# Kernel optimization log

Measured on AMD Instinct MI355X. Metric: run time of the kernel, lower is better.

Reference implementation:

```python
import jax, jax.numpy as jnp
import numpy as np

N_AUTHOR, N_PAPER = 20000, 50000
E = 300000
D, H = 256, 8
DK = D // H  # 32


def setup_inputs() -> dict:
    key = jax.random.key(0)
    ks = jax.random.split(key, 20)
    s = np.float32(1.0 / np.sqrt(D))
    sr = np.float32(1.0 / np.sqrt(DK))
    inp = {
        "h_author": jax.random.normal(ks[0], (N_AUTHOR, D), jnp.float32),
        "h_paper": jax.random.normal(ks[1], (N_PAPER, D), jnp.float32),
        "k_w": jax.random.normal(ks[2], (2, D, D), jnp.float32) * s,
        "k_b": jnp.zeros((2, D), jnp.float32),
        "q_w": jax.random.normal(ks[3], (2, D, D), jnp.float32) * s,
        "q_b": jnp.zeros((2, D), jnp.float32),
        "v_w": jax.random.normal(ks[4], (2, D, D), jnp.float32) * s,
        "v_b": jnp.zeros((2, D), jnp.float32),
        "a_w": jax.random.normal(ks[5], (2, D, D), jnp.float32) * s,
        "a_b": jnp.zeros((2, D), jnp.float32),
        "rel_att": jax.random.normal(ks[6], (3, H, DK, DK), jnp.float32) * sr,
        "rel_msg": jax.random.normal(ks[7], (3, H, DK, DK), jnp.float32) * sr,
        "rel_pri": jnp.ones((3, H), jnp.float32),
        "skip": jnp.ones((2,), jnp.float32),
        "src_writes": jax.random.randint(ks[8], (E,), 0, N_AUTHOR),
        "dst_writes": jax.random.randint(ks[9], (E,), 0, N_PAPER),
        "src_cites": jax.random.randint(ks[10], (E,), 0, N_PAPER),
        "dst_cites": jax.random.randint(ks[11], (E,), 0, N_PAPER),
        "src_wb": jax.random.randint(ks[12], (E,), 0, N_PAPER),
        "dst_wb": jax.random.randint(ks[13], (E,), 0, N_AUTHOR),
    }
    return inp


def _seg_softmax(score, seg, n):
    # dst-normalized edge softmax (per-etype subgraph, like DGL edge_softmax)
    m = jax.ops.segment_max(score, seg, num_segments=n)
    m = jnp.where(jnp.isfinite(m), m, 0.0)
    a = jnp.exp(score - m[seg])
    s = jax.ops.segment_sum(a, seg, num_segments=n)
    return a / s[seg]


def _etype_agg(h_src, h_dst, kw, kb, qw, qb, vw, vb, ratt, rmsg, pri, src, dst, n_dst):
    k = (h_src @ kw.T + kb).reshape(-1, H, DK)
    v = (h_src @ vw.T + vb).reshape(-1, H, DK)
    q = (h_dst @ qw.T + qb).reshape(-1, H, DK)
    k = jnp.einsum('nhi,hij->nhj', k, ratt)
    v = jnp.einsum('nhi,hij->nhj', v, rmsg)
    score = (q[dst] * k[src]).sum(-1) * pri / np.float32(np.sqrt(DK))  # [E,H]
    attn = _seg_softmax(score, dst, n_dst)
    return jax.ops.segment_sum(v[src] * attn[:, :, None], dst, num_segments=n_dst)


def reference(h_author, h_paper, k_w, k_b, q_w, q_b, v_w, v_b, a_w, a_b,
              rel_att, rel_msg, rel_pri, skip,
              src_writes, dst_writes, src_cites, dst_cites, src_wb, dst_wb):
    # ntypes: author=0, paper=1; etypes: writes=0 (a->p), cites=1 (p->p), written_by=2 (p->a)
    agg_p = _etype_agg(h_author, h_paper, k_w[0], k_b[0], q_w[1], q_b[1], v_w[0], v_b[0],
                       rel_att[0], rel_msg[0], rel_pri[0], src_writes, dst_writes, N_PAPER)
    agg_p = agg_p + _etype_agg(h_paper, h_paper, k_w[1], k_b[1], q_w[1], q_b[1], v_w[1], v_b[1],
                               rel_att[1], rel_msg[1], rel_pri[1], src_cites, dst_cites, N_PAPER)
    agg_a = _etype_agg(h_paper, h_author, k_w[1], k_b[1], q_w[0], q_b[0], v_w[1], v_b[1],
                       rel_att[2], rel_msg[2], rel_pri[2], src_wb, dst_wb, N_AUTHOR)

    def out_block(agg, h, nid):
        alpha = jax.nn.sigmoid(skip[nid])
        trans = agg.reshape(-1, D) @ a_w[nid].T + a_b[nid]
        return trans * alpha + h * (1.0 - alpha)

    return (out_block(agg_a, h_author, 0), out_block(agg_p, h_paper, 1))
```

## Files before the change

### kernel.cpp

```cpp
#include <hip/hip_runtime.h>
#include <hip/hip_bf16.h>

#define NA 20000
#define NP 50000
#define NE 300000
#define DD 256
#define HH 8
#define NTOT (2 * NP + NA)
#define NBLK ((NTOT + 2047) / 2048)
#define NRT 391

typedef short bf16x8 __attribute__((ext_vector_type(8)));
typedef float f32x4 __attribute__((ext_vector_type(4)));

__device__ __forceinline__ float b2f(ushort u) {
  unsigned v = ((unsigned)u) << 16;
  float f;
  __builtin_memcpy(&f, &v, 4);
  return f;
}
__device__ __forceinline__ float b2f_lo(int u) {
  unsigned v = ((unsigned)u) << 16;
  float f;
  __builtin_memcpy(&f, &v, 4);
  return f;
}
__device__ __forceinline__ float b2f_hi(int u) {
  unsigned v = ((unsigned)u) & 0xffff0000u;
  float f;
  __builtin_memcpy(&f, &v, 4);
  return f;
}
__device__ __forceinline__ ushort f2b(float f) {
  unsigned u;
  __builtin_memcpy(&u, &f, 4);
  u = u + 0x7fffu + ((u >> 16) & 1u);
  return (ushort)(u >> 16);
}
__device__ __forceinline__ unsigned pk2(float lo, float hi) {
  return (unsigned)f2b(lo) | ((unsigned)f2b(hi) << 16);
}
__device__ __forceinline__ float ldf(const void* p, int i, int isbf) {
  return isbf ? b2f(((const ushort*)p)[i]) : ((const float*)p)[i];
}
__device__ __forceinline__ int get_isbf(const void* rpri) {
  return ((const unsigned*)rpri)[0] == 0x3F803F80u;
}
__device__ __forceinline__ void gload16(const void* g, void* l) {
  __builtin_amdgcn_global_load_lds(
      (const __attribute__((address_space(1))) void*)g,
      (__attribute__((address_space(3))) void*)l, 16, 0, 0);
}

__global__ __launch_bounds__(256) void cvt_h(const void* __restrict__ ha,
                                             const void* __restrict__ hp,
                                             ushort* __restrict__ Ha,
                                             ushort* __restrict__ Hp,
                                             const void* __restrict__ rpri) {
  int isbf = get_isbf(rpri);
  size_t t = (size_t)blockIdx.x * 256 + threadIdx.x;
  const size_t nA = (size_t)NA * 256 / 8;
  const size_t nT = nA + (size_t)NP * 256 / 8;
  if (t >= nT) return;
  const void* src;
  ushort* dst;
  size_t o;
  if (t < nA) { src = ha; dst = Ha; o = t * 8; }
  else        { src = hp; dst = Hp; o = (t - nA) * 8; }
  if (isbf) {
    *(int4*)(dst + o) = *(const int4*)((const ushort*)src + o);
  } else {
    const float* f = (const float*)src + o;
    float4 x = *(const float4*)f;
    float4 y = *(const float4*)(f + 4);
    int4 v;
    v.x = (int)pk2(x.x, x.y); v.y = (int)pk2(x.z, x.w);
    v.z = (int)pk2(y.x, y.y); v.w = (int)pk2(y.z, y.w);
    *(int4*)(dst + o) = v;
  }
}

__global__ __launch_bounds__(256) void prep(const void* __restrict__ q_w,
                                            const void* __restrict__ a_w,
                                            const void* __restrict__ k_w,
                                            const void* __restrict__ v_w,
                                            const void* __restrict__ k_b,
                                            const void* __restrict__ v_b,
                                            const void* __restrict__ q_b,
                                            const void* __restrict__ ratt,
                                            const void* __restrict__ rmsg,
                                            ushort* __restrict__ Bp,
                                            ushort* __restrict__ Ba,
                                            ushort* __restrict__ aeff,
                                            float* __restrict__ gb,
                                            const void* __restrict__ rpri) {
  int isbf = get_isbf(rpri);
  int y = blockIdx.y;
  int r = blockIdx.x;
  int c = threadIdx.x;
  if (y < 3) {
    int e = y;
    int nt = (e == 2) ? 0 : 1;
    int h = r >> 5, i = r & 31;
    int rb = ((e * HH + h) * 32 + i) * 32;
    int qb = nt * 65536 + (h * 32) * 256 + c;
    float s = 0.f;
#pragma unroll 8
    for (int j = 0; j < 32; j++) s += ldf(ratt, rb + j, isbf) * ldf(q_w, qb + j * 256, isbf);
    ushort* dst = (e == 2) ? (Ba + (size_t)(512 + r) * 256)
                           : (Bp + (size_t)(512 + e * 256 + r) * 256);
    dst[c] = f2b(s);
  } else if (y < 6) {
    int e = y - 3;
    int o = r;
    int nt = (e == 2) ? 0 : 1;
    int h = c >> 5, i = c & 31;
    int rb = ((e * HH + h) * 32 + i) * 32;
    int ab = nt * 65536 + o * 256 + h * 32;
    float s = 0.f;
#pragma unroll 8
    for (int j = 0; j < 32; j++) s += ldf(rmsg, rb + j, isbf) * ldf(a_w, ab + j, isbf);
    aeff[(e * 256 + o) * 256 + c] = f2b(s);
  } else if (r < 128) {
    int t = r * 256 + c;
    int sec = t >> 13;
    int o = (t & 8191) * 8;
    const void* src = (sec == 0 || sec == 2) ? k_w : v_w;
    size_t soff = (sec < 2) ? (size_t)(65536 + o) : (size_t)o;
    ushort* dst = (sec == 0) ? (Bp + o)
                : (sec == 1) ? (Bp + 65536 + o)
                : (sec == 2) ? (Ba + o)
                             : (Ba + 65536 + o);
    if (isbf) {
      *(int4*)dst = *(const int4*)((const ushort*)src + soff);
    } else {
      const float* f = (const float*)src + soff;
      float4 x = *(const float4*)f;
      float4 yy = *(const float4*)(f + 4);
      int4 v;
      v.x = (int)pk2(x.x, x.y); v.y = (int)pk2(x.z, x.w);
      v.z = (int)pk2(yy.x, yy.y); v.w = (int)pk2(yy.z, yy.w);
      *(int4*)dst = v;
    }
  } else if (r == 128) {
    gb[0 * 256 + c] = ldf(k_b, 256 + c, isbf);
    gb[1 * 256 + c] = ldf(v_b, 256 + c, isbf);
    gb[4 * 256 + c] = ldf(k_b, c, isbf);
    gb[5 * 256 + c] = ldf(v_b, c, isbf);
    int h = c >> 5, i = c & 31;
    for (int e = 0; e < 3; e++) {
      int ntp = (e == 2) ? 0 : 1;
      int rb = ((e * HH + h) * 32 + i) * 32;
      float s = 0.f;
      for (int j = 0; j < 32; j++)
        s += ldf(ratt, rb + j, isbf) * ldf(q_b, ntp * 256 + h * 32 + j, isbf);
      gb[(e == 2 ? 6 : (2 + e)) * 256 + c] = s;
    }
  }
}

struct GemmC4 { ushort* c[4]; int ilv[4]; };

__global__ __launch_bounds__(256) void gemm_proj(const ushort* __restrict__ Hp,
                                                 const ushort* __restrict__ Ha,
                                                 const ushort* __restrict__ Bpp,
                                                 const ushort* __restrict__ Bap,
                                                 const float* __restrict__ gb,
                                                 GemmC4 cpp, GemmC4 cpa) {
  const int bid = blockIdx.x;
  const int xcd = bid & 7, seq = bid >> 3;
  const int rt = (seq / 14) * 8 + xcd;
  const int y = seq % 14;
  if (rt >= NRT) return;
  const int isNP = (y < 8);
  const int M = isNP ? NP : NA;
  const int row0 = rt * 128;
  if (row0 >= M) return;
  const ushort* A = isNP ? Hp : Ha;
  const ushort* B = isNP ? Bpp : Bap;
  const float* gbias = isNP ? gb : (gb + 1024);
  const int col0 = (isNP ? y : (y - 8)) * 128;
  const GemmC4 cp = isNP ? cpp : cpa;
  ushort* C = cp.c[col0 >> 8];
  const int ilv = cp.ilv[col0 >> 8];
  const int ccol0 = col0 & 255;

  __shared__ __align__(16) ushort As[2][4096];
  __shared__ __align__(16) ushort Bs[2][4096];
  const int tid = threadIdx.x;
  const int ln = tid & 63, wv = tid >> 6;
  const int quad = ln >> 4, lr = ln & 15;
  const int wr = wv >> 1, wc = wv & 1;

  f32x4 acc[4][4];
#pragma unroll
  for (int m = 0; m < 4; m++)
#pragma unroll
    for (int n = 0; n < 4; n++) acc[m][n] = (f32x4){0.f, 0.f, 0.f, 0.f};

  const int r0 = tid >> 2, seg = tid & 3;
  const int r1 = 64 + r0;
  int ar0 = row0 + r0; if (ar0 >= M) ar0 = M - 1;
  int ar1 = row0 + r1; if (ar1 >= M) ar1 = M - 1;
  const ushort* gA0 = A + ((size_t)ar0 * 256 + seg * 8);
  const ushort* gA1 = A + ((size_t)ar1 * 256 + seg * 8);
  const ushort* gB0 = B + ((size_t)(col0 + r0) * 256 + seg * 8);
  const ushort* gB1 = B + ((size_t)(col0 + r1) * 256 + seg * 8);
  const int lbase = (tid & 192) * 8;

  auto stage = [&](int kb, int buf) {
    gload16(gA0 + kb * 32, As[buf] + lbase);
    gload16(gA1 + kb * 32, As[buf] + 2048 + lbase);
    gload16(gB0 + kb * 32, Bs[buf] + lbase);
    gload16(gB1 + kb * 32, Bs[buf] + 2048 + lbase);
  };

  stage(0, 0);
  __syncthreads();
  for (int kb = 0; kb < 8; kb++) {
    const int cur = kb & 1;
    if (kb < 7) stage(kb + 1, cur ^ 1);
    bf16x8 af[4], bfr[4];
#pragma unroll
    for (int m = 0; m < 4; m++)
      af[m] = *(const bf16x8*)&As[cur][(wr * 64 + m * 16 + lr) * 32 + quad * 8];
#pragma unroll
    for (int n = 0; n < 4; n++)
      bfr[n] = *(const bf16x8*)&Bs[cur][(wc * 64 + n * 16 + lr) * 32 + quad * 8];
#pragma unroll
    for (int m = 0; m < 4; m++)
#pragma unroll
      for (int n = 0; n < 4; n++)
        acc[m][n] = __builtin_amdgcn_mfma_f32_16x16x32_bf16(bfr[n], af[m], acc[m][n], 0, 0, 0);
    __syncthreads();
  }

  const int voff = (ilv == 2) ? 4 : 0;
#pragma unroll
  for (int m = 0; m < 4; m++) {
    int row = row0 + wr * 64 + m * 16 + lr;
    if (row >= M) continue;
#pragma unroll
    for (int n = 0; n < 4; n++) {
      int ccol = ccol0 + wc * 64 + n * 16 + quad * 4;
      int gcol = col0 + wc * 64 + n * 16 + quad * 4;
      float4 bv = *(const float4*)(gbias + gcol);
      ushort4 o;
      o.x = f2b(acc[m][n][0] + bv.x);
      o.y = f2b(acc[m][n][1] + bv.y);
      o.z = f2b(acc[m][n][2] + bv.z);
      o.w = f2b(acc[m][n][3] + bv.w);
      size_t cidx = ilv ? ((size_t)row * 512 + (size_t)(ccol >> 2) * 8 + voff)
                        : ((size_t)row * 256 + ccol);
      *(ushort4*)(C + cidx) = o;
    }
  }
}

__global__ __launch_bounds__(256) void out_gemm2(const ushort* __restrict__ Aa,
                                                 const ushort* __restrict__ Ba_,
                                                 const ushort* __restrict__ Ap0,
                                                 const ushort* __restrict__ Bp0,
                                                 const ushort* __restrict__ Ap1,
                                                 const ushort* __restrict__ Bp1,
                                                 const void* __restrict__ ab,
                                                 const void* __restrict__ h_a,
                                                 const void* __restrict__ h_p,
                                                 const void* __restrict__ skipv,
                                                 void* __restrict__ out,
                                                 const void* __restrict__ rpri) {
  const int y = blockIdx.y;
  const int isA = (y < 2);
  const int M = isA ? NA : NP;
  const int row0 = blockIdx.x * 128;
  if (row0 >= M) return;
  const ushort* A0 = isA ? Aa : Ap0;
  const ushort* B0 = isA ? Ba_ : Bp0;
  const ushort* A1 = isA ? nullptr : Ap1;
  const ushort* B1 = isA ? nullptr : Bp1;
  const int ab_off = isA ? 0 : 256;
  const void* h = isA ? h_a : h_p;
  const int skipidx = isA ? 0 : 1;
  const size_t out_off = isA ? 0 : (size_t)NA * DD;
  const int col0 = (isA ? y : (y - 2)) * 128;

  const int isbf = get_isbf(rpri);
  __shared__ __align__(16) ushort As[2][4096];
  __shared__ __align__(16) ushort Bs[2][4096];
  const int tid = threadIdx.x;
  const int ln = tid & 63, wv = tid >> 6;
  const int quad = ln >> 4, lr = ln & 15;
  const int wr = wv >> 1, wc = wv & 1;

  f32x4 acc[4][4];
#pragma unroll
  for (int m = 0; m < 4; m++)
#pragma unroll
    for (int n = 0; n < 4; n++) acc[m][n] = (f32x4){0.f, 0.f, 0.f, 0.f};

  const int r0 = tid >> 2, seg = tid & 3;
  const int r1 = 64 + r0;
  int ar0 = row0 + r0; if (ar0 >= M) ar0 = M - 1;
  int ar1 = row0 + r1; if (ar1 >= M) ar1 = M - 1;
  const int lbase = (tid & 192) * 8;

  const int nsteps = (A1 != nullptr) ? 16 : 8;
  auto stage = [&](int s, int buf) {
    int g = s >> 3, kb = s & 7;
    const ushort* A = g ? A1 : A0;
    const ushort* B = g ? B1 : B0;
    gload16(A + (size_t)ar0 * 256 + seg * 8 + kb * 32, As[buf] + lbase);
    gload16(A + (size_t)ar1 * 256 + seg * 8 + kb * 32, As[buf] + 2048 + lbase);
    gload16(B + (size_t)(col0 + r0) * 256 + seg * 8 + kb * 32, Bs[buf] + lbase);
    gload16(B + (size_t)(col0 + r1) * 256 + seg * 8 + kb * 32, Bs[buf] + 2048 + lbase);
  };

  stage(0, 0);
  __syncthreads();
  for (int s = 0; s < nsteps; s++) {
    const int cur = s & 1;
    if (s + 1 < nsteps) stage(s + 1, cur ^ 1);
    bf16x8 af[4], bfr[4];
#pragma unroll
    for (int m = 0; m < 4; m++)
      af[m] = *(const bf16x8*)&As[cur][(wr * 64 + m * 16 + lr) * 32 + quad * 8];
#pragma unroll
    for (int n = 0; n < 4; n++)
      bfr[n] = *(const bf16x8*)&Bs[cur][(wc * 64 + n * 16 + lr) * 32 + quad * 8];
#pragma unroll
    for (int m = 0; m < 4; m++)
#pragma unroll
      for (int n = 0; n < 4; n++)
        acc[m][n] = __builtin_amdgcn_mfma_f32_16x16x32_bf16(bfr[n], af[m], acc[m][n], 0, 0, 0);
    __syncthreads();
  }

  float alpha = 1.f / (1.f + __expf(-ldf(skipv, skipidx, isbf)));
  float beta = 1.f - alpha;
#pragma unroll
  for (int m = 0; m < 4; m++) {
    int row = row0 + wr * 64 + m * 16 + lr;
    if (row >= M) continue;
#pragma unroll
    for (int n = 0; n < 4; n++) {
      int col = col0 + wc * 64 + n * 16 + quad * 4;
      size_t base = (size_t)row * 256 + col;
      float t0 = acc[m][n][0] + ldf(ab, ab_off + col + 0, isbf);
      float t1 = acc[m][n][1] + ldf(ab, ab_off + col + 1, isbf);
      float t2 = acc[m][n][2] + ldf(ab, ab_off + col + 2, isbf);
      float t3 = acc[m][n][3] + ldf(ab, ab_off + col + 3, isbf);
      if (isbf) {
        ushort4 hu = *(const ushort4*)((const ushort*)h + base);
        ushort4 o;
        o.x = f2b(alpha * t0 + beta * b2f(hu.x));
        o.y = f2b(alpha * t1 + beta * b2f(hu.y));
        o.z = f2b(alpha * t2 + beta * b2f(hu.z));
        o.w = f2b(alpha * t3 + beta * b2f(hu.w));
        *(ushort4*)((ushort*)out + out_off + base) = o;
      } else {
        float4 hf = *(const float4*)((const float*)h + base);
        float4 o;
        o.x = alpha * t0 + beta * hf.x;
        o.y = alpha * t1 + beta * hf.y;
        o.z = alpha * t2 + beta * hf.z;
        o.w = alpha * t3 + beta * hf.w;
        *(float4*)((float*)out + out_off + base) = o;
      }
    }
  }
}

__global__ void count_edges(const int* __restrict__ d0, const int* __restrict__ d1,
                            const int* __restrict__ d2, int* __restrict__ cnt) {
  int i = blockIdx.x * 256 + threadIdx.x;
  if (i >= 3 * NE) return;
  int et = (i >= 2 * NE) ? 2 : ((i >= NE) ? 1 : 0);
  int e = i - et * NE;
  const int* dd = (et == 0) ? d0 : ((et == 1) ? d1 : d2);
  int base = (et == 0) ? 0 : ((et == 1) ? NP : 2 * NP);
  atomicAdd(&cnt[base + dd[e]], 1);
}

__global__ __launch_bounds__(256) void reduce_cnt(const int* __restrict__ cnt,
                                                  int* __restrict__ bsum) {
  __shared__ int red[256];
  int t = threadIdx.x;
  int base = blockIdx.x * 2048 + t * 8;
  int s = 0;
#pragma unroll
  for (int j = 0; j < 8; j++) s += (base + j < NTOT) ? cnt[base + j] : 0;
  red[t] = s;
  __syncthreads();
  for (int o = 128; o > 0; o >>= 1) {
    if (t < o) red[t] += red[t + o];
    __syncthreads();
  }
  if (t == 0) bsum[blockIdx.x] = red[0];
}

__global__ __launch_bounds__(64) void scan_top(const int* __restrict__ bsum,
                                               int* __restrict__ ebase) {
  __shared__ int ts[64];
  int t = threadIdx.x;
  int v = (t < NBLK) ? bsum[t] : 0;
  ts[t] = v;
  __syncthreads();
  for (int o = 1; o < 64; o <<= 1) {
    int x = (t >= o) ? ts[t - o] : 0;
    __syncthreads();
    ts[t] += x;
    __syncthreads();
  }
  if (t < NBLK) ebase[t] = ts[t] - v;
}

__global__ __launch_bounds__(256) void scan_final(const int* __restrict__ cnt,
                                                  const int* __restrict__ ebase,
                                                  int* __restrict__ offs,
                                                  int* __restrict__ cur) {
  __shared__ int ts[256];
  int t = threadIdx.x;
  int base = blockIdx.x * 2048 + t * 8;
  int v[8];
  int s = 0;
#pragma unroll
  for (int j = 0; j < 8; j++) {
    int x = (base + j < NTOT) ? cnt[base + j] : 0;
    v[j] = s;
    s += x;
  }
  ts[t] = s;
  __syncthreads();
  for (int o = 1; o < 256; o <<= 1) {
    int x = (t >= o) ? ts[t - o] : 0;
    __syncthreads();
    ts[t] += x;
    __syncthreads();
  }
  int tb = ebase[blockIdx.x] + ts[t] - s;
#pragma unroll
  for (int j = 0; j < 8; j++) {
    int i = base + j;
    if (i < NTOT) {
      int o2 = tb + v[j];
      offs[i] = o2;
      cur[i] = o2;
    }
  }
  if (blockIdx.x == 0 && t == 0) offs[NTOT] = 3 * NE;
}

__global__ void scatter_edges(const int* __restrict__ s0, const int* __restrict__ d0,
                              const int* __restrict__ s1, const int* __restrict__ d1,
                              const int* __restrict__ s2, const int* __restrict__ d2,
                              int* __restrict__ cur, int* __restrict__ csr) {
  int i = blockIdx.x * 256 + threadIdx.x;
  if (i >= 3 * NE) return;
  int et = (i >= 2 * NE) ? 2 : ((i >= NE) ? 1 : 0);
  int e = i - et * NE;
  const int* ss = (et == 0) ? s0 : ((et == 1) ? s1 : s2);
  const int* dd = (et == 0) ? d0 : ((et == 1) ? d1 : d2);
  int base = (et == 0) ? 0 : ((et == 1) ? NP : 2 * NP);
  int pos = atomicAdd(&cur[base + dd[e]], 1);
  csr[pos] = ss[e];
}

__global__ __launch_bounds__(256) void edge_agg_all(ushort* __restrict__ Qe0,
                                                    ushort* __restrict__ Qe1,
                                                    ushort* __restrict__ Qe2,
                                                    const ushort* __restrict__ KVa,
                                                    const ushort* __restrict__ KVp,
                                                    const int* __restrict__ offs,
                                                    const int* __restrict__ csr,
                                                    const void* __restrict__ pri) {
  int isbf = get_isbf(pri);
  int wv = threadIdx.x >> 6;
  int g = blockIdx.x * 4 + wv;
  if (g >= NTOT) return;
  int ln = threadIdx.x & 63;
  int h = ln >> 3;
  int d, pri_off, n_src;
  ushort* Q;
  const ushort* KV;
  if (g < NP) {
    d = g; Q = Qe0; KV = KVa; pri_off = 0; n_src = NA;
  } else if (g < 2 * NP) {
    d = g - NP; Q = Qe1; KV = KVp; pri_off = 8; n_src = NP;
  } else {
    d = g - 2 * NP; Q = Qe2; KV = KVp; pri_off = 16; n_src = NP;
  }
  float prif = ldf(pri, pri_off + h, isbf) * 0.17677669529663687f;
  ushort4 qu = *(const ushort4*)(Q + (size_t)d * 256 + ln * 4);
  float q0 = b2f(qu.x) * prif, q1 = b2f(qu.y) * prif;
  float q2 = b2f(qu.z) * prif, q3 = b2f(qu.w) * prif;
  float m = -1e30f, l = 0.f;
  float a0 = 0.f, a1 = 0.f, a2 = 0.f, a3 = 0.f;
  int e0 = __builtin_amdgcn_readfirstlane(offs[g]);
  int e1 = __builtin_amdgcn_readfirstlane(offs[g + 1]);
  if (e1 > e0 + 4096) e1 = e0 + 4096;

  for (int e = e0; e < e1; e += 8) {
    int nv = e1 - e;
    nv = (nv > 8) ? 8 : nv;
    int4 kv[8];
    float sc[8];
#pragma unroll
    for (int i = 0; i < 8; i++) sc[i] = -1e30f;
#pragma unroll
    for (int i = 0; i < 8; i++) {
      if (i < nv) {
        unsigned s = (unsigned)csr[e + i];
        if (s >= (unsigned)n_src) s = 0;
        kv[i] = *(const int4*)(KV + (size_t)s * 512 + ln * 8);
      }
    }
#pragma unroll
    for (int i = 0; i < 8; i++) {
      if (i < nv) {
        float p = q0 * b2f_lo(kv[i].x) + q1 * b2f_hi(kv[i].x) +
                  q2 * b2f_lo(kv[i].y) + q3 * b2f_hi(kv[i].y);
        p += __shfl_xor(p, 1);
        p += __shfl_xor(p, 2);
        p += __shfl_xor(p, 4);
        sc[i] = p;
      }
    }
    float mc = fmaxf(fmaxf(fmaxf(sc[0], sc[1]), fmaxf(sc[2], sc[3])),
                     fmaxf(fmaxf(sc[4], sc[5]), fmaxf(sc[6], sc[7])));
    float mn = fmaxf(m, mc);
    if (e != e0) {
      float scale = __expf(m - mn);
      l *= scale; a0 *= scale; a1 *= scale; a2 *= scale; a3 *= scale;
    }
#pragma unroll
    for (int i = 0; i < 8; i++) {
      if (i < nv) {
        float wgt = __expf(sc[i] - mn);
        l += wgt;
        a0 += wgt * b2f_lo(kv[i].z);
        a1 += wgt * b2f_hi(kv[i].z);
        a2 += wgt * b2f_lo(kv[i].w);
        a3 += wgt * b2f_hi(kv[i].w);
      }
    }
    m = mn;
  }
  float inv = (l > 0.f) ? 1.f / l : 0.f;
  ushort4 o;
  o.x = f2b(a0 * inv);
  o.y = f2b(a1 * inv);
  o.z = f2b(a2 * inv);
  o.w = f2b(a3 * inv);
  *(ushort4*)(Q + (size_t)d * 256 + ln * 4) = o;
}

extern "C" void kernel_launch(void* const* d_in, const int* in_sizes, int n_in,
                              void* d_out, int out_size, void* d_ws, size_t ws_size,
                              hipStream_t stream) {
  (void)in_sizes; (void)n_in; (void)out_size; (void)ws_size;
  const void* h_a = d_in[0];
  const void* h_p = d_in[1];
  const void* k_w = d_in[2];
  const void* k_b = d_in[3];
  const void* q_w = d_in[4];
  const void* q_b = d_in[5];
  const void* v_w = d_in[6];
  const void* v_b = d_in[7];
  const void* a_w = d_in[8];
  const void* a_b = d_in[9];
  const void* ratt = d_in[10];
  const void* rmsg = d_in[11];
  const void* rpri = d_in[12];
  const void* skip = d_in[13];
  const int* src_w = (const int*)d_in[14];
  const int* dst_w = (const int*)d_in[15];
  const int* src_c = (const int*)d_in[16];
  const int* dst_c = (const int*)d_in[17];
  const int* src_b = (const int*)d_in[18];
  const int* dst_b = (const int*)d_in[19];

  char* w = (char*)d_ws;
  size_t ofs = 0;
  auto alloc = [&](size_t bytes) {
    char* p = w + ofs;
    ofs = (ofs + bytes + 255) & ~(size_t)255;
    return p;
  };
  ushort* Bp = (ushort*)alloc((size_t)1024 * 256 * 2);
  ushort* Ba = (ushort*)alloc((size_t)768 * 256 * 2);
  ushort* aeff = (ushort*)alloc((size_t)3 * 256 * 256 * 2);
  float* gb = (float*)alloc((size_t)7 * 256 * 4);
  int* cnt = (int*)alloc((size_t)NTOT * 4);
  int* offs = (int*)alloc((size_t)(NTOT + 1) * 4);
  int* bsum = (int*)alloc(64 * 4);
  int* ebase = (int*)alloc(64 * 4);
  int* cur = (int*)alloc((size_t)NTOT * 4);
  int* csr = (int*)alloc((size_t)3 * NE * 4);
  ushort* Ha = (ushort*)alloc((size_t)NA * DD * 2);
  ushort* Hp = (ushort*)alloc((size_t)NP * DD * 2);
  ushort* KVa = (ushort*)alloc((size_t)NA * 512 * 2);
  ushort* KVp = (ushort*)alloc((size_t)NP * 512 * 2);
  ushort* Qe0 = (ushort*)alloc((size_t)NP * DD * 2);
  ushort* Qe1 = (ushort*)alloc((size_t)NP * DD * 2);
  ushort* Qe2 = (ushort*)alloc((size_t)NA * DD * 2);
  ushort* agg0 = Qe0;
  ushort* agg1 = Qe1;
  ushort* agg2 = Qe2;

  hipMemsetAsync(cnt, 0, (size_t)NTOT * 4, stream);

  cvt_h<<<(2240000 + 255) / 256, 256, 0, stream>>>(h_a, h_p, Ha, Hp, rpri);
  prep<<<dim3(256, 7), 256, 0, stream>>>(q_w, a_w, k_w, v_w, k_b, v_b, q_b,
                                         ratt, rmsg, Bp, Ba, aeff, gb, rpri);

  GemmC4 cpp, cpa;
  cpp.c[0] = KVp; cpp.ilv[0] = 1;
  cpp.c[1] = KVp; cpp.ilv[1] = 2;
  cpp.c[2] = Qe0; cpp.ilv[2] = 0;
  cpp.c[3] = Qe1; cpp.ilv[3] = 0;
  cpa.c[0] = KVa; cpa.ilv[0] = 1;
  cpa.c[1] = KVa; cpa.ilv[1] = 2;
  cpa.c[2] = Qe2; cpa.ilv[2] = 0;
  cpa.c[3] = Qe2; cpa.ilv[3] = 0;
  gemm_proj<<<8 * 50 * 14, 256, 0, stream>>>(Hp, Ha, Bp, Ba, gb, cpp, cpa);

  count_edges<<<(3 * NE + 255) / 256, 256, 0, stream>>>(dst_w, dst_c, dst_b, cnt);
  reduce_cnt<<<NBLK, 256, 0, stream>>>(cnt, bsum);
  scan_top<<<1, 64, 0, stream>>>(bsum, ebase);
  scan_final<<<NBLK, 256, 0, stream>>>(cnt, ebase, offs, cur);
  scatter_edges<<<(3 * NE + 255) / 256, 256, 0, stream>>>(src_w, dst_w, src_c, dst_c,
                                                          src_b, dst_b, cur, csr);

  edge_agg_all<<<(NTOT + 3) / 4, 256, 0, stream>>>(Qe0, Qe1, Qe2, KVa, KVp,
                                                   offs, csr, rpri);

  out_gemm2<<<dim3((NP + 127) / 128, 4), 256, 0, stream>>>(
      agg2, aeff + 131072, agg0, aeff, agg1, aeff + 65536,
      a_b, h_a, h_p, skip, d_out, rpri);
}
```

Baseline: 583.0 us.

## Fuse independent stages into shared launches and make edge aggregation branch-free

Merges bf16 conversion, weight prep and edge counting into one launch, and merges the projection GEMM with the CSR scatter into another, so independent work shares a grid and two launch gaps go away. The scan kernels now run before the projection GEMM. Separately, the edge aggregation loop drops its per-edge validity branches. It clamps the index to the last edge, reads the source id with readfirstlane, and masks the scores with -1e30. The cost is that the GEMM blocks now share the device with atomic-heavy scatter blocks, and padded lanes issue redundant loads.

Result: faster. 541.6 us (-7.1%).

```diff
diff --git a/kernel.cpp b/kernel.cpp
--- a/kernel.cpp
+++ b/kernel.cpp
@@ -10,6 +10,12 @@
 #define NBLK ((NTOT + 2047) / 2048)
 #define NRT 391
 
+#define CVT_B 8750
+#define PREP_B 1792
+#define CNT_B 3516
+#define PROJ_B (8 * 50 * 14)
+#define SCAT_B 3516
+
 typedef short bf16x8 __attribute__((ext_vector_type(8)));
 typedef float f32x4 __attribute__((ext_vector_type(4)));
 
@@ -52,122 +58,157 @@
       (__attribute__((address_space(3))) void*)l, 16, 0, 0);
 }
 
-__global__ __launch_bounds__(256) void cvt_h(const void* __restrict__ ha,
-                                             const void* __restrict__ hp,
-                                             ushort* __restrict__ Ha,
-                                             ushort* __restrict__ Hp,
-                                             const void* __restrict__ rpri) {
-  int isbf = get_isbf(rpri);
-  size_t t = (size_t)blockIdx.x * 256 + threadIdx.x;
-  const size_t nA = (size_t)NA * 256 / 8;
-  const size_t nT = nA + (size_t)NP * 256 / 8;
-  if (t >= nT) return;
-  const void* src;
-  ushort* dst;
-  size_t o;
-  if (t < nA) { src = ha; dst = Ha; o = t * 8; }
-  else        { src = hp; dst = Hp; o = (t - nA) * 8; }
-  if (isbf) {
-    *(int4*)(dst + o) = *(const int4*)((const ushort*)src + o);
-  } else {
-    const float* f = (const float*)src + o;
-    float4 x = *(const float4*)f;
-    float4 y = *(const float4*)(f + 4);
-    int4 v;
-    v.x = (int)pk2(x.x, x.y); v.y = (int)pk2(x.z, x.w);
-    v.z = (int)pk2(y.x, y.y); v.w = (int)pk2(y.z, y.w);
-    *(int4*)(dst + o) = v;
-  }
-}
-
-__global__ __launch_bounds__(256) void prep(const void* __restrict__ q_w,
-                                            const void* __restrict__ a_w,
-                                            const void* __restrict__ k_w,
-                                            const void* __restrict__ v_w,
-                                            const void* __restrict__ k_b,
-                                            const void* __restrict__ v_b,
-                                            const void* __restrict__ q_b,
-                                            const void* __restrict__ ratt,
-                                            const void* __restrict__ rmsg,
-                                            ushort* __restrict__ Bp,
-                                            ushort* __restrict__ Ba,
-                                            ushort* __restrict__ aeff,
-                                            float* __restrict__ gb,
-                                            const void* __restrict__ rpri) {
-  int isbf = get_isbf(rpri);
-  int y = blockIdx.y;
-  int r = blockIdx.x;
-  int c = threadIdx.x;
-  if (y < 3) {
-    int e = y;
-    int nt = (e == 2) ? 0 : 1;
-    int h = r >> 5, i = r & 31;
-    int rb = ((e * HH + h) * 32 + i) * 32;
-    int qb = nt * 65536 + (h * 32) * 256 + c;
-    float s = 0.f;
-#pragma unroll 8
-    for (int j = 0; j < 32; j++) s += ldf(ratt, rb + j, isbf) * ldf(q_w, qb + j * 256, isbf);
-    ushort* dst = (e == 2) ? (Ba + (size_t)(512 + r) * 256)
-                           : (Bp + (size_t)(512 + e * 256 + r) * 256);
-    dst[c] = f2b(s);
-  } else if (y < 6) {
-    int e = y - 3;
-    int o = r;
-    int nt = (e == 2) ? 0 : 1;
-    int h = c >> 5, i = c & 31;
-    int rb = ((e * HH + h) * 32 + i) * 32;
-    int ab = nt * 65536 + o * 256 + h * 32;
-    float s = 0.f;
-#pragma unroll 8
-    for (int j = 0; j < 32; j++) s += ldf(rmsg, rb + j, isbf) * ldf(a_w, ab + j, isbf);
-    aeff[(e * 256 + o) * 256 + c] = f2b(s);
-  } else if (r < 128) {
-    int t = r * 256 + c;
-    int sec = t >> 13;
-    int o = (t & 8191) * 8;
-    const void* src = (sec == 0 || sec == 2) ? k_w : v_w;
-    size_t soff = (sec < 2) ? (size_t)(65536 + o) : (size_t)o;
-    ushort* dst = (sec == 0) ? (Bp + o)
-                : (sec == 1) ? (Bp + 65536 + o)
-                : (sec == 2) ? (Ba + o)
-                             : (Ba + 65536 + o);
+__global__ __launch_bounds__(256) void phase0(const void* __restrict__ ha,
+                                              const void* __restrict__ hp,
+                                              ushort* __restrict__ Ha,
+                                              ushort* __restrict__ Hp,
+                                              const void* __restrict__ q_w,
+                                              const void* __restrict__ a_w,
+                                              const void* __restrict__ k_w,
+                                              const void* __restrict__ v_w,
+                                              const void* __restrict__ k_b,
+                                              const void* __restrict__ v_b,
+                                              const void* __restrict__ q_b,
+                                              const void* __restrict__ ratt,
+                                              const void* __restrict__ rmsg,
+                                              ushort* __restrict__ Bp,
+                                              ushort* __restrict__ Ba,
+                                              ushort* __restrict__ aeff,
+                                              float* __restrict__ gb,
+                                              const int* __restrict__ d0,
+                                              const int* __restrict__ d1,
+                                              const int* __restrict__ d2,
+                                              int* __restrict__ cnt,
+                                              const void* __restrict__ rpri) {
+  const int b = blockIdx.x;
+  const int c = threadIdx.x;
+  const int isbf = get_isbf(rpri);
+  if (b < CVT_B) {
+    size_t t = (size_t)b * 256 + c;
+    const size_t nA = (size_t)NA * 256 / 8;
+    const size_t nT = nA + (size_t)NP * 256 / 8;
+    if (t >= nT) return;
+    const void* src;
+    ushort* dst;
+    size_t o;
+    if (t < nA) { src = ha; dst = Ha; o = t * 8; }
+    else        { src = hp; dst = Hp; o = (t - nA) * 8; }
     if (isbf) {
-      *(int4*)dst = *(const int4*)((const ushort*)src + soff);
+      *(int4*)(dst + o) = *(const int4*)((const ushort*)src + o);
     } else {
-      const float* f = (const float*)src + soff;
+      const float* f = (const float*)src + o;
       float4 x = *(const float4*)f;
-      float4 yy = *(const float4*)(f + 4);
+      float4 y = *(const float4*)(f + 4);
       int4 v;
       v.x = (int)pk2(x.x, x.y); v.y = (int)pk2(x.z, x.w);
-      v.z = (int)pk2(yy.x, yy.y); v.w = (int)pk2(yy.z, yy.w);
-      *(int4*)dst = v;
-    }
-  } else if (r == 128) {
-    gb[0 * 256 + c] = ldf(k_b, 256 + c, isbf);
-    gb[1 * 256 + c] = ldf(v_b, 256 + c, isbf);
-    gb[4 * 256 + c] = ldf(k_b, c, isbf);
-    gb[5 * 256 + c] = ldf(v_b, c, isbf);
-    int h = c >> 5, i = c & 31;
-    for (int e = 0; e < 3; e++) {
-      int ntp = (e == 2) ? 0 : 1;
+      v.z = (int)pk2(y.x, y.y); v.w = (int)pk2(y.z, y.w);
+      *(int4*)(dst + o) = v;
+    }
+  } else if (b < CVT_B + PREP_B) {
+    int pid = b - CVT_B;
+    int y = pid >> 8;
+    int r = pid & 255;
+    if (y < 3) {
+      int e = y;
+      int nt = (e == 2) ? 0 : 1;
+      int h = r >> 5, i = r & 31;
       int rb = ((e * HH + h) * 32 + i) * 32;
+      int qb = nt * 65536 + (h * 32) * 256 + c;
       float s = 0.f;
-      for (int j = 0; j < 32; j++)
-        s += ldf(ratt, rb + j, isbf) * ldf(q_b, ntp * 256 + h * 32 + j, isbf);
-      gb[(e == 2 ? 6 : (2 + e)) * 256 + c] = s;
-    }
+#pragma unroll 8
+      for (int j = 0; j < 32; j++) s += ldf(ratt, rb + j, isbf) * ldf(q_w, qb + j * 256, isbf);
+      ushort* dst = (e == 2) ? (Ba + (size_t)(512 + r) * 256)
+                             : (Bp + (size_t)(512 + e * 256 + r) * 256);
+      dst[c] = f2b(s);
+    } else if (y < 6) {
+      int e = y - 3;
+      int o = r;
+      int nt = (e == 2) ? 0 : 1;
+      int h = c >> 5, i = c & 31;
+      int rb = ((e * HH + h) * 32 + i) * 32;
+      int ab = nt * 65536 + o * 256 + h * 32;
+      float s = 0.f;
+#pragma unroll 8
+      for (int j = 0; j < 32; j++) s += ldf(rmsg, rb + j, isbf) * ldf(a_w, ab + j, isbf);
+      aeff[(e * 256 + o) * 256 + c] = f2b(s);
+    } else if (r < 128) {
+      int t = r * 256 + c;
+      int sec = t >> 13;
+      int o = (t & 8191) * 8;
+      const void* src = (sec == 0 || sec == 2) ? k_w : v_w;
+      size_t soff = (sec < 2) ? (size_t)(65536 + o) : (size_t)o;
+      ushort* dst = (sec == 0) ? (Bp + o)
+                  : (sec == 1) ? (Bp + 65536 + o)
+                  : (sec == 2) ? (Ba + o)
+                               : (Ba + 65536 + o);
+      if (isbf) {
+        *(int4*)dst = *(const int4*)((const ushort*)src + soff);
+      } else {
+        const float* f = (const float*)src + soff;
+        float4 x = *(const float4*)f;
+        float4 yy = *(const float4*)(f + 4);
+        int4 v;
+        v.x = (int)pk2(x.x, x.y); v.y = (int)pk2(x.z, x.w);
+        v.z = (int)pk2(yy.x, yy.y); v.w = (int)pk2(yy.z, yy.w);
+        *(int4*)dst = v;
+      }
+    } else if (r == 128) {
+      gb[0 * 256 + c] = ldf(k_b, 256 + c, isbf);
+      gb[1 * 256 + c] = ldf(v_b, 256 + c, isbf);
+      gb[4 * 256 + c] = ldf(k_b, c, isbf);
+      gb[5 * 256 + c] = ldf(v_b, c, isbf);
+      int h = c >> 5, i = c & 31;
+      for (int e = 0; e < 3; e++) {
+        int ntp = (e == 2) ? 0 : 1;
+        int rb = ((e * HH + h) * 32 + i) * 32;
+        float s = 0.f;
+        for (int j = 0; j < 32; j++)
+          s += ldf(ratt, rb + j, isbf) * ldf(q_b, ntp * 256 + h * 32 + j, isbf);
+        gb[(e == 2 ? 6 : (2 + e)) * 256 + c] = s;
+      }
+    }
+  } else {
+    int i = (b - CVT_B - PREP_B) * 256 + c;
+    if (i >= 3 * NE) return;
+    int et = (i >= 2 * NE) ? 2 : ((i >= NE) ? 1 : 0);
+    int e = i - et * NE;
+    const int* dd = (et == 0) ? d0 : ((et == 1) ? d1 : d2);
+    int base = (et == 0) ? 0 : ((et == 1) ? NP : 2 * NP);
+    atomicAdd(&cnt[base + dd[e]], 1);
   }
 }
 
 struct GemmC4 { ushort* c[4]; int ilv[4]; };
 
-__global__ __launch_bounds__(256) void gemm_proj(const ushort* __restrict__ Hp,
-                                                 const ushort* __restrict__ Ha,
-                                                 const ushort* __restrict__ Bpp,
-                                                 const ushort* __restrict__ Bap,
-                                                 const float* __restrict__ gb,
-                                                 GemmC4 cpp, GemmC4 cpa) {
+__global__ __launch_bounds__(256) void proj_scatter(const ushort* __restrict__ Hp,
+                                                    const ushort* __restrict__ Ha,
+                                                    const ushort* __restrict__ Bpp,
+                                                    const ushort* __restrict__ Bap,
+                                                    const float* __restrict__ gb,
+                                                    GemmC4 cpp, GemmC4 cpa,
+                                                    const int* __restrict__ s0,
+                                                    const int* __restrict__ d0,
+                                                    const int* __restrict__ s1,
+                                                    const int* __restrict__ d1,
+                                                    const int* __restrict__ s2,
+                                                    const int* __restrict__ d2,
+                                                    int* __restrict__ cur,
+                                                    int* __restrict__ csr) {
+  __shared__ __align__(16) ushort As[2][4096];
+  __shared__ __align__(16) ushort Bs[2][4096];
   const int bid = blockIdx.x;
+  if (bid >= PROJ_B) {
+    int i = (bid - PROJ_B) * 256 + threadIdx.x;
+    if (i >= 3 * NE) return;
+    int et = (i >= 2 * NE) ? 2 : ((i >= NE) ? 1 : 0);
+    int e = i - et * NE;
+    const int* ss = (et == 0) ? s0 : ((et == 1) ? s1 : s2);
+    const int* dd = (et == 0) ? d0 : ((et == 1) ? d1 : d2);
+    int base = (et == 0) ? 0 : ((et == 1) ? NP : 2 * NP);
+    int pos = atomicAdd(&cur[base + dd[e]], 1);
+    csr[pos] = ss[e];
+    return;
+  }
   const int xcd = bid & 7, seq = bid >> 3;
   const int rt = (seq / 14) * 8 + xcd;
   const int y = seq % 14;
@@ -185,8 +226,6 @@
   const int ilv = cp.ilv[col0 >> 8];
   const int ccol0 = col0 & 255;
 
-  __shared__ __align__(16) ushort As[2][4096];
-  __shared__ __align__(16) ushort Bs[2][4096];
   const int tid = threadIdx.x;
   const int ln = tid & 63, wv = tid >> 6;
   const int quad = ln >> 4, lr = ln & 15;
@@ -218,15 +257,15 @@
   stage(0, 0);
   __syncthreads();
   for (int kb = 0; kb < 8; kb++) {
-    const int cur = kb & 1;
-    if (kb < 7) stage(kb + 1, cur ^ 1);
+    const int cur_ = kb & 1;
+    if (kb < 7) stage(kb + 1, cur_ ^ 1);
     bf16x8 af[4], bfr[4];
 #pragma unroll
     for (int m = 0; m < 4; m++)
-      af[m] = *(const bf16x8*)&As[cur][(wr * 64 + m * 16 + lr) * 32 + quad * 8];
+      af[m] = *(const bf16x8*)&As[cur_][(wr * 64 + m * 16 + lr) * 32 + quad * 8];
 #pragma unroll
     for (int n = 0; n < 4; n++)
-      bfr[n] = *(const bf16x8*)&Bs[cur][(wc * 64 + n * 16 + lr) * 32 + quad * 8];
+      bfr[n] = *(const bf16x8*)&Bs[cur_][(wc * 64 + n * 16 + lr) * 32 + quad * 8];
 #pragma unroll
     for (int m = 0; m < 4; m++)
 #pragma unroll
@@ -318,15 +357,15 @@
   stage(0, 0);
   __syncthreads();
   for (int s = 0; s < nsteps; s++) {
-    const int cur = s & 1;
-    if (s + 1 < nsteps) stage(s + 1, cur ^ 1);
+    const int cur_ = s & 1;
+    if (s + 1 < nsteps) stage(s + 1, cur_ ^ 1);
     bf16x8 af[4], bfr[4];
 #pragma unroll
     for (int m = 0; m < 4; m++)
-      af[m] = *(const bf16x8*)&As[cur][(wr * 64 + m * 16 + lr) * 32 + quad * 8];
+      af[m] = *(const bf16x8*)&As[cur_][(wr * 64 + m * 16 + lr) * 32 + quad * 8];
 #pragma unroll
     for (int n = 0; n < 4; n++)
-      bfr[n] = *(const bf16x8*)&Bs[cur][(wc * 64 + n * 16 + lr) * 32 + quad * 8];
+      bfr[n] = *(const bf16x8*)&Bs[cur_][(wc * 64 + n * 16 + lr) * 32 + quad * 8];
 #pragma unroll
     for (int m = 0; m < 4; m++)
 #pragma unroll
@@ -370,17 +409,6 @@
   }
 }
 
-__global__ void count_edges(const int* __restrict__ d0, const int* __restrict__ d1,
-                            const int* __restrict__ d2, int* __restrict__ cnt) {
-  int i = blockIdx.x * 256 + threadIdx.x;
-  if (i >= 3 * NE) return;
-  int et = (i >= 2 * NE) ? 2 : ((i >= NE) ? 1 : 0);
-  int e = i - et * NE;
-  const int* dd = (et == 0) ? d0 : ((et == 1) ? d1 : d2);
-  int base = (et == 0) ? 0 : ((et == 1) ? NP : 2 * NP);
-  atomicAdd(&cnt[base + dd[e]], 1);
-}
-
 __global__ __launch_bounds__(256) void reduce_cnt(const int* __restrict__ cnt,
                                                   int* __restrict__ bsum) {
   __shared__ int red[256];
@@ -448,21 +476,6 @@
     }
   }
   if (blockIdx.x == 0 && t == 0) offs[NTOT] = 3 * NE;
-}
-
-__global__ void scatter_edges(const int* __restrict__ s0, const int* __restrict__ d0,
-                              const int* __restrict__ s1, const int* __restrict__ d1,
-                              const int* __restrict__ s2, const int* __restrict__ d2,
-                              int* __restrict__ cur, int* __restrict__ csr) {
-  int i = blockIdx.x * 256 + threadIdx.x;
-  if (i >= 3 * NE) return;
-  int et = (i >= 2 * NE) ? 2 : ((i >= NE) ? 1 : 0);
-  int e = i - et * NE;
-  const int* ss = (et == 0) ? s0 : ((et == 1) ? s1 : s2);
-  const int* dd = (et == 0) ? d0 : ((et == 1) ? d1 : d2);
-  int base = (et == 0) ? 0 : ((et == 1) ? NP : 2 * NP);
-  int pos = atomicAdd(&cur[base + dd[e]], 1);
-  csr[pos] = ss[e];
 }
 
 __global__ __launch_bounds__(256) void edge_agg_all(ushort* __restrict__ Qe0,
@@ -498,6 +511,7 @@
   int e0 = __builtin_amdgcn_readfirstlane(offs[g]);
   int e1 = __builtin_amdgcn_readfirstlane(offs[g + 1]);
   if (e1 > e0 + 4096) e1 = e0 + 4096;
+  const int elast = e1 - 1;
 
   for (int e = e0; e < e1; e += 8) {
     int nv = e1 - e;
@@ -505,25 +519,21 @@
     int4 kv[8];
     float sc[8];
 #pragma unroll
-    for (int i = 0; i < 8; i++) sc[i] = -1e30f;
-#pragma unroll
     for (int i = 0; i < 8; i++) {
-      if (i < nv) {
-        unsigned s = (unsigned)csr[e + i];
-        if (s >= (unsigned)n_src) s = 0;
-        kv[i] = *(const int4*)(KV + (size_t)s * 512 + ln * 8);
-      }
+      int idx = e + i;
+      idx = (idx > elast) ? elast : idx;
+      unsigned s = (unsigned)__builtin_amdgcn_readfirstlane(csr[idx]);
+      if (s >= (unsigned)n_src) s = 0;
+      kv[i] = *(const int4*)(KV + (size_t)s * 512 + ln * 8);
     }
 #pragma unroll
     for (int i = 0; i < 8; i++) {
-      if (i < nv) {
-        float p = q0 * b2f_lo(kv[i].x) + q1 * b2f_hi(kv[i].x) +
-                  q2 * b2f_lo(kv[i].y) + q3 * b2f_hi(kv[i].y);
-        p += __shfl_xor(p, 1);
-        p += __shfl_xor(p, 2);
-        p += __shfl_xor(p, 4);
-        sc[i] = p;
-      }
+      float p = q0 * b2f_lo(kv[i].x) + q1 * b2f_hi(kv[i].x) +
+                q2 * b2f_lo(kv[i].y) + q3 * b2f_hi(kv[i].y);
+      p += __shfl_xor(p, 1);
+      p += __shfl_xor(p, 2);
+      p += __shfl_xor(p, 4);
+      sc[i] = (i < nv) ? p : -1e30f;
     }
     float mc = fmaxf(fmaxf(fmaxf(sc[0], sc[1]), fmaxf(sc[2], sc[3])),
                      fmaxf(fmaxf(sc[4], sc[5]), fmaxf(sc[6], sc[7])));
@@ -534,14 +544,12 @@
     }
 #pragma unroll
     for (int i = 0; i < 8; i++) {
-      if (i < nv) {
-        float wgt = __expf(sc[i] - mn);
-        l += wgt;
-        a0 += wgt * b2f_lo(kv[i].z);
-        a1 += wgt * b2f_hi(kv[i].z);
-        a2 += wgt * b2f_lo(kv[i].w);
-        a3 += wgt * b2f_hi(kv[i].w);
-      }
+      float wgt = __expf(sc[i] - mn);
+      l += wgt;
+      a0 += wgt * b2f_lo(kv[i].z);
+      a1 += wgt * b2f_hi(kv[i].z);
+      a2 += wgt * b2f_lo(kv[i].w);
+      a3 += wgt * b2f_hi(kv[i].w);
     }
     m = mn;
   }
@@ -609,9 +617,13 @@
 
   hipMemsetAsync(cnt, 0, (size_t)NTOT * 4, stream);
 
-  cvt_h<<<(2240000 + 255) / 256, 256, 0, stream>>>(h_a, h_p, Ha, Hp, rpri);
-  prep<<<dim3(256, 7), 256, 0, stream>>>(q_w, a_w, k_w, v_w, k_b, v_b, q_b,
-                                         ratt, rmsg, Bp, Ba, aeff, gb, rpri);
+  phase0<<<CVT_B + PREP_B + CNT_B, 256, 0, stream>>>(
+      h_a, h_p, Ha, Hp, q_w, a_w, k_w, v_w, k_b, v_b, q_b, ratt, rmsg,
+      Bp, Ba, aeff, gb, dst_w, dst_c, dst_b, cnt, rpri);
+
+  reduce_cnt<<<NBLK, 256, 0, stream>>>(cnt, bsum);
+  scan_top<<<1, 64, 0, stream>>>(bsum, ebase);
+  scan_final<<<NBLK, 256, 0, stream>>>(cnt, ebase, offs, cur);
 
   GemmC4 cpp, cpa;
   cpp.c[0] = KVp; cpp.ilv[0] = 1;
@@ -622,14 +634,9 @@
   cpa.c[1] = KVa; cpa.ilv[1] = 2;
   cpa.c[2] = Qe2; cpa.ilv[2] = 0;
   cpa.c[3] = Qe2; cpa.ilv[3] = 0;
-  gemm_proj<<<8 * 50 * 14, 256, 0, stream>>>(Hp, Ha, Bp, Ba, gb, cpp, cpa);
-
-  count_edges<<<(3 * NE + 255) / 256, 256, 0, stream>>>(dst_w, dst_c, dst_b, cnt);
-  reduce_cnt<<<NBLK, 256, 0, stream>>>(cnt, bsum);
-  scan_top<<<1, 64, 0, stream>>>(bsum, ebase);
-  scan_final<<<NBLK, 256, 0, stream>>>(cnt, ebase, offs, cur);
-  scatter_edges<<<(3 * NE + 255) / 256, 256, 0, stream>>>(src_w, dst_w, src_c, dst_c,
-                                                          src_b, dst_b, cur, csr);
+  proj_scatter<<<PROJ_B + SCAT_B, 256, 0, stream>>>(
+      Hp, Ha, Bp, Ba, gb, cpp, cpa,
+      src_w, dst_w, src_c, dst_c, src_b, dst_b, cur, csr);
 
   edge_agg_all<<<(NTOT + 3) / 4, 256, 0, stream>>>(Qe0, Qe1, Qe2, KVa, KVp,
                                                    offs, csr, rpri);
```
